# Kernel optimization log

Hardware: AMD Instinct MI355X
Metric: run time of the kernel (lower is better)

The kernel has to match this reference:

```python
import jax, jax.numpy as jnp
import numpy as np

G = 8
K = 3  # kernel size; Unfold uses padding=1, stride=1 -> output same HxW


def _unfold3x3(x):
    # x: (b, c, h, w) -> (b, c, K*K, h, w), patch order (kh, kw) matching torch Unfold
    b, c, h, w = x.shape
    xp = jnp.pad(x, ((0, 0), (0, 0), (1, 1), (1, 1)))
    patches = [xp[:, :, i:i + h, j:j + w] for i in range(K) for j in range(K)]
    return jnp.stack(patches, axis=2)


def setup_inputs() -> dict:
    key = jax.random.key(0)
    k1, k2, k3, k4, k5 = jax.random.split(key, 5)
    b, c, h, w = 16, 256, 56, 56
    r = 2
    return {
        "x": jax.random.normal(k1, (b, c, h, w), dtype=jnp.float32),
        "w_reduce": jax.random.normal(k2, (c // r, c), dtype=jnp.float32) * (1.0 / np.sqrt(c)),
        "b_reduce": jax.random.normal(k3, (c // r,), dtype=jnp.float32) * 0.01,
        "w_span": jax.random.normal(k4, (K * K * G, c // r), dtype=jnp.float32) * (1.0 / np.sqrt(c // r)),
        "b_span": jax.random.normal(k5, (K * K * G,), dtype=jnp.float32) * 0.01,
    }


def reference(x, w_reduce, b_reduce, w_span, b_span):
    b, c, h, w = x.shape
    kk = K * K
    # dynamic kernel: two 1x1 convs (ss=1 -> no pooling)
    red = jnp.einsum('bchw,oc->bohw', x, w_reduce) + b_reduce[None, :, None, None]
    ker = jnp.einsum('bohw,ko->bkhw', red, w_span) + b_span[None, :, None, None]
    ker = ker.reshape(b, G, kk, h, w)
    # unfold: (b, c, kk, h, w) -> (b, G, c//G, kk, h, w)
    xu = _unfold3x3(x).reshape(b, G, c // G, kk, h, w)
    # broadcast-mul and reduce over kernel positions
    out = jnp.einsum('bgkhw,bgdkhw->bgdhw', ker, xu)
    return out.reshape(b, c, h, w)
```

## Files before the change

kernel.cpp:

```cpp
#include <hip/hip_runtime.h>
#include <hip/hip_bf16.h>

#define HW 3136
#define CC 256
#define MM 72
#define HH 56
#define WW 56

typedef __attribute__((ext_vector_type(8))) short short8;
typedef __attribute__((ext_vector_type(4))) float f32x4;

#define WAITVM(n) asm volatile("s_waitcnt vmcnt(" #n ")" ::: "memory")

__device__ __forceinline__ void blockbar() {
    asm volatile("" ::: "memory");
    __builtin_amdgcn_s_barrier();
    asm volatile("" ::: "memory");
}

__device__ inline unsigned short f2b(float f) {
    unsigned u; __builtin_memcpy(&u, &f, 4);
    unsigned r = u + 0x7fffu + ((u >> 16) & 1u);
    return (unsigned short)(r >> 16);
}
__device__ inline float b2f(unsigned short s) {
    unsigned u = ((unsigned)s) << 16; float f; __builtin_memcpy(&f, &u, 4);
    return f;
}
__device__ __forceinline__ unsigned short f2b_native(float f) {
    __hip_bfloat16 h = __float2bfloat16(f);
    unsigned short s; __builtin_memcpy(&s, &h, 2);
    return s;
}

__device__ __forceinline__ void gl2lds16(const float* g, float* l) {
    __builtin_amdgcn_global_load_lds(
        (const __attribute__((address_space(1))) void*)g,
        (__attribute__((address_space(3))) void*)l, 16, 0, 0);
}

__global__ __launch_bounds__(256) void k0_combine(
    const float* __restrict__ w_reduce,
    const float* __restrict__ b_reduce,
    const float* __restrict__ w_span,
    const float* __restrict__ b_span,
    unsigned short* __restrict__ wbf,
    float* __restrict__ bcomb)
{
    __shared__ float red[4][64];
    __shared__ float redb[256];

    const int m  = blockIdx.x;
    const int cq = blockIdx.y;
    const int t  = threadIdx.x;
    const int oq = t >> 6;
    const int cl = t & 63;
    const int c  = cq * 64 + cl;

    float acc = 0.f;
    if (m < MM) {
        const float* wsB = w_span   + m * 128 + oq * 32;
        const float* wrB = w_reduce + (size_t)(oq * 32) * 256 + c;
#pragma unroll 8
        for (int o = 0; o < 32; ++o)
            acc = fmaf(wsB[o], wrB[(size_t)o * 256], acc);
    }
    if (oq != 0) red[oq][cl] = acc;
    __syncthreads();
    if (oq == 0)
        wbf[m * 256 + c] = f2b(acc + red[1][cl] + red[2][cl] + red[3][cl]);

    if (cq == 0) {
        redb[t] = (m < MM && t < 128) ? w_span[m * 128 + t] * b_reduce[t] : 0.f;
        __syncthreads();
#pragma unroll
        for (int s2 = 128; s2 > 0; s2 >>= 1) {
            if (t < s2) redb[t] += redb[t + s2];
            __syncthreads();
        }
        if (t == 0) bcomb[m] = (m < MM ? b_span[m] : 0.f) + redb[0];
    }
}

__global__ __launch_bounds__(448, 4) void k_fused(
    const float* __restrict__ x,
    const unsigned short* __restrict__ wbf,
    const float* __restrict__ bcomb,
    float* __restrict__ out)
{
    __shared__ __align__(16) float xsb[13824];
    __shared__ __align__(16) unsigned short wsl[2][2560];
    __shared__ __align__(16) unsigned short kl[MM * 112];

    const int L   = blockIdx.x;
    const int wk  = (L & 7) * 56 + (L >> 3);
    const int b   = wk / 28;
    const int rem = wk - b * 28;
    const int ht  = rem >> 1;
    const int cs  = rem & 1;
    const int h0  = ht * 4;
    const int c0  = cs * 28;

    const int t    = threadIdx.x;
    const int lane = t & 63;
    const int wv   = t >> 6;
    const int l15  = lane & 15;
    const int q    = lane >> 4;

    const int chh   = t / 28;
    const int rem28 = t - chh * 28;
    const int rA    = rem28 / 7;
    const int qA    = rem28 - rA * 7;

    const float* xb = x + (size_t)b * CC * HW;

    const int nb   = wv * 16 + l15;
    const int nb2  = q * 112 + nb;
    const int swA  = (l15 ^ (l15 >> 2)) & 3;
    const int aBo  = l15 * 32 + (q ^ swA) * 8;
    const int cA   = ((chh & 3) << 3) | (chh >> 2);
    const int pxo  = (h0 + rA) * WW + c0 + qA * 4;
    const int wswr = ((t >> 2) ^ (t >> 4)) & 3;
    const unsigned short* wsrc0 = wbf + (t >> 2) * 256 + ((t & 3) ^ wswr) * 8;

    int aoffv[4], bdst[4];
#pragma unroll
    for (int i = 0; i < 4; ++i) {
        int f = i * 448 + t;
        if (f >= 1728) f -= 448;
        const int d  = f / 54;
        const int r2 = f - d * 54;
        const int rr = r2 / 9;
        const int qd = r2 - rr * 9;
        const int hh = h0 - 1 + rr;
        const int hc = hh < 0 ? 0 : (hh > 55 ? 55 : hh);
        int colc = c0 - 4 + qd * 4;
        colc = colc < 0 ? 0 : (colc > 52 ? 52 : colc);
        aoffv[i] = d * HW + hc * WW + colc;
        bdst[i]  = f * 4;
    }

    float vmm[3];
#pragma unroll
    for (int kh = 0; kh < 3; ++kh) {
        const int row = h0 + rA - 1 + kh;
        vmm[kh] = (row >= 0 && row < HH) ? 1.f : 0.f;
    }
    const float lm  = (cs == 0 && qA == 0) ? 0.f : 1.f;
    const float rmm = (cs == 1 && qA == 6) ? 0.f : 1.f;

    auto stageX = [&](int s, int p) {
        const float* sp = xb + (size_t)(s * 32 + cA) * HW + pxo;
        float* dp = xsb + p * 6912 + t * 4;
        gl2lds16(sp, dp);
        gl2lds16(sp + (size_t)4 * HW, dp + 1792);
    };
    auto stageW = [&](int s, int p) {
        if (t < 320)
            gl2lds16((const float*)(wsrc0 + s * 32), (float*)(wsl[p]) + t * 4);
    };
    auto stageB = [&](int g, int p) {
        const float* gp = xb + (size_t)g * 32 * HW;
        float* dp = xsb + p * 6912;
#pragma unroll
        for (int i = 0; i < 4; ++i)
            gl2lds16(gp + aoffv[i], dp + bdst[i]);
    };

    f32x4 acc[5];
#pragma unroll
    for (int mt = 0; mt < 5; ++mt)
#pragma unroll
        for (int r = 0; r < 4; ++r)
            acc[mt][r] = bcomb[mt * 16 + q * 4 + r];

    stageX(0, 0); stageW(0, 0);
    stageX(1, 1); stageW(1, 1);

#pragma unroll 1
    for (int s = 0; s < 8; ++s) {
        const int p = s & 1;
        if (s < 7) { if (t < 320) WAITVM(3); else WAITVM(2); }
        else       { WAITVM(4); }
        blockbar();

        const float* bufA = xsb + p * 6912;
        const unsigned short* wp = wsl[p];
        union { short8 v; unsigned short u16[8]; } bq;
#pragma unroll
        for (int j = 0; j < 8; ++j)
            bq.u16[j] = f2b_native(bufA[nb2 + j * 448]);
#pragma unroll
        for (int mt = 0; mt < 5; ++mt) {
            const short8 aq = *(const short8*)&wp[mt * 512 + aBo];
            acc[mt] = __builtin_amdgcn_mfma_f32_16x16x32_bf16(aq, bq.v, acc[mt], 0, 0, 0);
        }
        if (s == 7) {
#pragma unroll
            for (int mt = 0; mt < 5; ++mt)
#pragma unroll
                for (int r = 0; r < 4; ++r) {
                    const int m = mt * 16 + q * 4 + r;
                    if (m < MM) kl[m * 112 + nb] = f2b(acc[mt][r]);
                }
            asm volatile("s_waitcnt lgkmcnt(0)" ::: "memory");
        }
        blockbar();
        if (s < 6) { stageX(s + 2, p); stageW(s + 2, p); }
        else       { stageB(s - 6, p); }
    }

#pragma unroll 1
    for (int g = 0; g < 8; ++g) {
        const int p = g & 1;
        if (g == 0)      WAITVM(4);
        else if (g == 7) WAITVM(2);
        else             WAITVM(6);
        blockbar();

        ushort4 krb[9];
#pragma unroll
        for (int kk = 0; kk < 9; ++kk)
            krb[kk] = *(const ushort4*)&kl[(g * 9 + kk) * 112 + rA * 28 + qA * 4];

        f32x4 kr[9];
#pragma unroll
        for (int kh = 0; kh < 3; ++kh) {
#pragma unroll
            for (int j = 0; j < 3; ++j) {
                const int kk = kh * 3 + j;
                kr[kk].x = b2f(krb[kk].x) * vmm[kh];
                kr[kk].y = b2f(krb[kk].y) * vmm[kh];
                kr[kk].z = b2f(krb[kk].z) * vmm[kh];
                kr[kk].w = b2f(krb[kk].w) * vmm[kh];
            }
            kr[kh * 3 + 0].x *= lm;
            kr[kh * 3 + 2].w *= rmm;
        }

        const float* bp0 = xsb + p * 6912;
        float* ob = out + ((size_t)b * CC + g * 32 + chh * 2) * HW
                  + (h0 + rA) * WW + c0 + qA * 4;
#pragma unroll
        for (int dd = 0; dd < 2; ++dd) {
            const float* bp = bp0 + (chh * 2 + dd) * 216;
            f32x4 a = {0.f, 0.f, 0.f, 0.f};
#pragma unroll
            for (int kh = 0; kh < 3; ++kh) {
                const float* rowp = bp + (rA + kh) * 36;
                const f32x4 q0v = *(const f32x4*)(rowp + qA * 4);
                const f32x4 q1v = *(const f32x4*)(rowp + qA * 4 + 4);
                const float tl  = rowp[qA * 4 + 8];
                const float w0 = q0v.w, w1 = q1v.x, w2 = q1v.y,
                            w3 = q1v.z, w4 = q1v.w, w5 = tl;
                const f32x4 k0v = kr[kh * 3 + 0];
                const f32x4 k1v = kr[kh * 3 + 1];
                const f32x4 k2v = kr[kh * 3 + 2];
                a.x = fmaf(k0v.x, w0, a.x); a.y = fmaf(k0v.y, w1, a.y);
                a.z = fmaf(k0v.z, w2, a.z); a.w = fmaf(k0v.w, w3, a.w);
                a.x = fmaf(k1v.x, w1, a.x); a.y = fmaf(k1v.y, w2, a.y);
                a.z = fmaf(k1v.z, w3, a.z); a.w = fmaf(k1v.w, w4, a.w);
                a.x = fmaf(k2v.x, w2, a.x); a.y = fmaf(k2v.y, w3, a.y);
                a.z = fmaf(k2v.z, w4, a.z); a.w = fmaf(k2v.w, w5, a.w);
            }
            *(f32x4*)(ob + (size_t)dd * HW) = a;
        }

        blockbar();
        if (g < 6) stageB(g + 2, p);
    }
}

extern "C" void kernel_launch(void* const* d_in, const int* in_sizes, int n_in,
                              void* d_out, int out_size, void* d_ws, size_t ws_size,
                              hipStream_t stream) {
    const float* x        = (const float*)d_in[0];
    const float* w_reduce = (const float*)d_in[1];
    const float* b_reduce = (const float*)d_in[2];
    const float* w_span   = (const float*)d_in[3];
    const float* b_span   = (const float*)d_in[4];
    float* out = (float*)d_out;

    char* ws = (char*)d_ws;
    unsigned short* wbf   = (unsigned short*)ws;
    float*          bcomb = (float*)(ws + 40960);

    k0_combine<<<dim3(80, 4), 256, 0, stream>>>(w_reduce, b_reduce, w_span, b_span,
                                                wbf, bcomb);
    k_fused<<<dim3(448), 448, 0, stream>>>(x, wbf, bcomb, out);
}
```

Measured before the change: 37.04 us.

## Switch fused kernel to triple-buffered LDS pipeline with smaller stages

Replaces the two-stage double buffer with a three-slot ring of half-size LDS buffers. Both the MFMA reduction phase and the unfold-apply phase now prefetch three stages ahead, and the apply phase runs in 16-channel chunks instead of 32. The goal is to keep more global loads in flight per block and to shrink LDS per block, which can raise occupancy and hide latency. The cost is more barriers and iterations, plus finer-grained vmcnt bookkeeping that must be exactly right to stay correct.

```diff
diff --git a/kernel.cpp b/kernel.cpp
--- a/kernel.cpp
+++ b/kernel.cpp
@@ -88,8 +88,8 @@
     const float* __restrict__ bcomb,
     float* __restrict__ out)
 {
-    __shared__ __align__(16) float xsb[13824];
-    __shared__ __align__(16) unsigned short wsl[2][2560];
+    __shared__ __align__(16) float xsb[3 * 3584];
+    __shared__ __align__(16) unsigned short wsl[3][2560];
     __shared__ __align__(16) unsigned short kl[MM * 112];
 
     const int L   = blockIdx.x;
@@ -123,21 +123,20 @@
     const int wswr = ((t >> 2) ^ (t >> 4)) & 3;
     const unsigned short* wsrc0 = wbf + (t >> 2) * 256 + ((t & 3) ^ wswr) * 8;
 
-    int aoffv[4], bdst[4];
-#pragma unroll
-    for (int i = 0; i < 4; ++i) {
-        int f = i * 448 + t;
-        if (f >= 1728) f -= 448;
-        const int d  = f / 54;
-        const int r2 = f - d * 54;
+    int boff[2];
+#pragma unroll
+    for (int i = 0; i < 2; ++i) {
+        const int f  = i * 448 + t;
+        const int fc = f < 864 ? f : 863;
+        const int d  = fc / 54;
+        const int r2 = fc - d * 54;
         const int rr = r2 / 9;
         const int qd = r2 - rr * 9;
         const int hh = h0 - 1 + rr;
         const int hc = hh < 0 ? 0 : (hh > 55 ? 55 : hh);
         int colc = c0 - 4 + qd * 4;
         colc = colc < 0 ? 0 : (colc > 52 ? 52 : colc);
-        aoffv[i] = d * HW + hc * WW + colc;
-        bdst[i]  = f * 4;
+        boff[i] = d * HW + hc * WW + colc;
     }
 
     float vmm[3];
@@ -149,22 +148,21 @@
     const float lm  = (cs == 0 && qA == 0) ? 0.f : 1.f;
     const float rmm = (cs == 1 && qA == 6) ? 0.f : 1.f;
 
-    auto stageX = [&](int s, int p) {
+    auto stageX = [&](int s) {
         const float* sp = xb + (size_t)(s * 32 + cA) * HW + pxo;
-        float* dp = xsb + p * 6912 + t * 4;
+        float* dp = xsb + (s % 3) * 3584 + t * 4;
         gl2lds16(sp, dp);
         gl2lds16(sp + (size_t)4 * HW, dp + 1792);
     };
-    auto stageW = [&](int s, int p) {
+    auto stageW = [&](int s) {
         if (t < 320)
-            gl2lds16((const float*)(wsrc0 + s * 32), (float*)(wsl[p]) + t * 4);
+            gl2lds16((const float*)(wsrc0 + s * 32), (float*)(wsl[s % 3]) + t * 4);
     };
-    auto stageB = [&](int g, int p) {
-        const float* gp = xb + (size_t)g * 32 * HW;
-        float* dp = xsb + p * 6912;
-#pragma unroll
-        for (int i = 0; i < 4; ++i)
-            gl2lds16(gp + aoffv[i], dp + bdst[i]);
+    auto stageB = [&](int c) {
+        const float* gp = xb + (size_t)(c * 16) * HW;
+        float* dp = xsb + ((8 + c) % 3) * 3584;
+        gl2lds16(gp + boff[0], dp + t * 4);
+        gl2lds16(gp + boff[1], dp + (448 + t) * 4);
     };
 
     f32x4 acc[5];
@@ -174,18 +172,19 @@
         for (int r = 0; r < 4; ++r)
             acc[mt][r] = bcomb[mt * 16 + q * 4 + r];
 
-    stageX(0, 0); stageW(0, 0);
-    stageX(1, 1); stageW(1, 1);
+    stageX(0); stageW(0);
+    stageX(1); stageW(1);
+    stageX(2); stageW(2);
 
 #pragma unroll 1
-    for (int s = 0; s < 8; ++s) {
-        const int p = s & 1;
-        if (s < 7) { if (t < 320) WAITVM(3); else WAITVM(2); }
-        else       { WAITVM(4); }
-        blockbar();
-
-        const float* bufA = xsb + p * 6912;
-        const unsigned short* wp = wsl[p];
+    for (int p = 0; p < 8; ++p) {
+        if (p < 6)      { if (t < 320) WAITVM(6); else WAITVM(4); }
+        else if (p == 6){ if (t < 320) WAITVM(5); else WAITVM(4); }
+        else            { WAITVM(4); }
+        blockbar();
+
+        const float* bufA = xsb + (p % 3) * 3584;
+        const unsigned short* wp = wsl[p % 3];
         union { short8 v; unsigned short u16[8]; } bq;
 #pragma unroll
         for (int j = 0; j < 8; ++j)
@@ -195,7 +194,7 @@
             const short8 aq = *(const short8*)&wp[mt * 512 + aBo];
             acc[mt] = __builtin_amdgcn_mfma_f32_16x16x32_bf16(aq, bq.v, acc[mt], 0, 0, 0);
         }
-        if (s == 7) {
+        if (p == 7) {
 #pragma unroll
             for (int mt = 0; mt < 5; ++mt)
 #pragma unroll
@@ -206,68 +205,67 @@
             asm volatile("s_waitcnt lgkmcnt(0)" ::: "memory");
         }
         blockbar();
-        if (s < 6) { stageX(s + 2, p); stageW(s + 2, p); }
-        else       { stageB(s - 6, p); }
-    }
-
+        if (p <= 4) { stageX(p + 3); stageW(p + 3); }
+        else        { stageB(p - 5); }
+    }
+
+    f32x4 kr[9];
 #pragma unroll 1
-    for (int g = 0; g < 8; ++g) {
-        const int p = g & 1;
-        if (g == 0)      WAITVM(4);
-        else if (g == 7) WAITVM(2);
-        else             WAITVM(6);
-        blockbar();
-
-        ushort4 krb[9];
-#pragma unroll
-        for (int kk = 0; kk < 9; ++kk)
-            krb[kk] = *(const ushort4*)&kl[(g * 9 + kk) * 112 + rA * 28 + qA * 4];
-
-        f32x4 kr[9];
+    for (int g2 = 0; g2 < 16; ++g2) {
+        if (g2 == 0)       WAITVM(4);
+        else if (g2 == 1)  WAITVM(5);
+        else if (g2 <= 13) WAITVM(6);
+        else if (g2 == 14) WAITVM(4);
+        else               WAITVM(2);
+        blockbar();
+
+        if ((g2 & 1) == 0) {
+            const int g = g2 >> 1;
+            ushort4 krb[9];
+#pragma unroll
+            for (int kk = 0; kk < 9; ++kk)
+                krb[kk] = *(const ushort4*)&kl[(g * 9 + kk) * 112 + rA * 28 + qA * 4];
+#pragma unroll
+            for (int kh = 0; kh < 3; ++kh) {
+#pragma unroll
+                for (int j = 0; j < 3; ++j) {
+                    const int kk = kh * 3 + j;
+                    kr[kk].x = b2f(krb[kk].x) * vmm[kh];
+                    kr[kk].y = b2f(krb[kk].y) * vmm[kh];
+                    kr[kk].z = b2f(krb[kk].z) * vmm[kh];
+                    kr[kk].w = b2f(krb[kk].w) * vmm[kh];
+                }
+                kr[kh * 3 + 0].x *= lm;
+                kr[kh * 3 + 2].w *= rmm;
+            }
+        }
+
+        const float* bp = xsb + ((8 + g2) % 3) * 3584 + chh * 216;
+        f32x4 a = {0.f, 0.f, 0.f, 0.f};
 #pragma unroll
         for (int kh = 0; kh < 3; ++kh) {
-#pragma unroll
-            for (int j = 0; j < 3; ++j) {
-                const int kk = kh * 3 + j;
-                kr[kk].x = b2f(krb[kk].x) * vmm[kh];
-                kr[kk].y = b2f(krb[kk].y) * vmm[kh];
-                kr[kk].z = b2f(krb[kk].z) * vmm[kh];
-                kr[kk].w = b2f(krb[kk].w) * vmm[kh];
-            }
-            kr[kh * 3 + 0].x *= lm;
-            kr[kh * 3 + 2].w *= rmm;
-        }
-
-        const float* bp0 = xsb + p * 6912;
-        float* ob = out + ((size_t)b * CC + g * 32 + chh * 2) * HW
+            const float* rowp = bp + (rA + kh) * 36;
+            const f32x4 q0v = *(const f32x4*)(rowp + qA * 4);
+            const f32x4 q1v = *(const f32x4*)(rowp + qA * 4 + 4);
+            const float tl  = rowp[qA * 4 + 8];
+            const float w0 = q0v.w, w1 = q1v.x, w2 = q1v.y,
+                        w3 = q1v.z, w4 = q1v.w, w5 = tl;
+            const f32x4 k0v = kr[kh * 3 + 0];
+            const f32x4 k1v = kr[kh * 3 + 1];
+            const f32x4 k2v = kr[kh * 3 + 2];
+            a.x = fmaf(k0v.x, w0, a.x); a.y = fmaf(k0v.y, w1, a.y);
+            a.z = fmaf(k0v.z, w2, a.z); a.w = fmaf(k0v.w, w3, a.w);
+            a.x = fmaf(k1v.x, w1, a.x); a.y = fmaf(k1v.y, w2, a.y);
+            a.z = fmaf(k1v.z, w3, a.z); a.w = fmaf(k1v.w, w4, a.w);
+            a.x = fmaf(k2v.x, w2, a.x); a.y = fmaf(k2v.y, w3, a.y);
+            a.z = fmaf(k2v.z, w4, a.z); a.w = fmaf(k2v.w, w5, a.w);
+        }
+        float* ob = out + ((size_t)b * CC + g2 * 16 + chh) * HW
                   + (h0 + rA) * WW + c0 + qA * 4;
-#pragma unroll
-        for (int dd = 0; dd < 2; ++dd) {
-            const float* bp = bp0 + (chh * 2 + dd) * 216;
-            f32x4 a = {0.f, 0.f, 0.f, 0.f};
-#pragma unroll
-            for (int kh = 0; kh < 3; ++kh) {
-                const float* rowp = bp + (rA + kh) * 36;
-                const f32x4 q0v = *(const f32x4*)(rowp + qA * 4);
-                const f32x4 q1v = *(const f32x4*)(rowp + qA * 4 + 4);
-                const float tl  = rowp[qA * 4 + 8];
-                const float w0 = q0v.w, w1 = q1v.x, w2 = q1v.y,
-                            w3 = q1v.z, w4 = q1v.w, w5 = tl;
-                const f32x4 k0v = kr[kh * 3 + 0];
-                const f32x4 k1v = kr[kh * 3 + 1];
-                const f32x4 k2v = kr[kh * 3 + 2];
-                a.x = fmaf(k0v.x, w0, a.x); a.y = fmaf(k0v.y, w1, a.y);
-                a.z = fmaf(k0v.z, w2, a.z); a.w = fmaf(k0v.w, w3, a.w);
-                a.x = fmaf(k1v.x, w1, a.x); a.y = fmaf(k1v.y, w2, a.y);
-                a.z = fmaf(k1v.z, w3, a.z); a.w = fmaf(k1v.w, w4, a.w);
-                a.x = fmaf(k2v.x, w2, a.x); a.y = fmaf(k2v.y, w3, a.y);
-                a.z = fmaf(k2v.z, w4, a.z); a.w = fmaf(k2v.w, w5, a.w);
-            }
-            *(f32x4*)(ob + (size_t)dd * HW) = a;
-        }
-
-        blockbar();
-        if (g < 6) stageB(g + 2, p);
+        *(f32x4*)ob = a;
+
+        blockbar();
+        if (g2 <= 12) stageB(g2 + 3);
     }
 }
 
```

After: 38.82 us. 4.8% more time.
